# Kernel tuning notes

Measured on AMD Instinct MI355X. Metric: run time of the kernel, lower is better.

Reference implementation:

```python
import jax, jax.numpy as jnp
import numpy as np

N_NODES = 100000
N_EDGES = 1600000
DIM = 128


def setup_inputs() -> dict:
    key = jax.random.key(0)
    k1, k2, k3, k4 = jax.random.split(key, 4)
    x = jax.random.normal(k1, (N_NODES, DIM), dtype=jnp.float32)
    edge_index = jax.random.randint(k2, (2, N_EDGES), 0, N_NODES, dtype=jnp.int64)
    # PyG GCNConv params: Linear weight [out, in] (glorot) and bias [out] (zeros -> use small randn for a non-trivial grad path)
    W = jax.random.normal(k3, (DIM, DIM), dtype=jnp.float32) * (1.0 / np.sqrt(DIM))
    b = jax.random.normal(k4, (DIM,), dtype=jnp.float32) * 0.01
    return {"x": x, "edge_index": edge_index, "W": W, "b": b}


def reference(x, edge_index, W, b):
    # Faithful GCNConv: add self-loops, symmetric deg^-1/2 normalization,
    # linear transform, scatter-add aggregation, bias.
    N = x.shape[0]
    loop = jnp.arange(N, dtype=edge_index.dtype)
    src = jnp.concatenate([edge_index[0], loop])  # [E+N]
    dst = jnp.concatenate([edge_index[1], loop])  # [E+N]

    # degree (with self-loops) on destination nodes
    deg = jax.ops.segment_sum(jnp.ones_like(dst, dtype=x.dtype), dst, num_segments=N)
    dinv = jnp.where(deg > 0, jax.lax.rsqrt(deg), 0.0)
    norm = dinv[src] * dinv[dst]  # [E+N]

    x_lin = x @ W.T  # [N, dim] — PyG applies linear before propagate
    msg = x_lin[src] * norm[:, None]  # [E+N, dim] gather + scale
    out = jax.ops.segment_sum(msg, dst, num_segments=N)  # scatter-add aggregate
    return out + b
```

## Files before the change

### kernel.cpp

```cpp
#include <hip/hip_runtime.h>
#include <hip/hip_bf16.h>


#define DIM 128
#define BINSHIFT 8
#define BINSZ 256
#define NB 391
#define CAPB 8192
#define BUFCAP 40
#define SBLK 128
#define ROUND 2048
#define WSTRIDE 136

typedef __attribute__((ext_vector_type(8))) short short8;
typedef __attribute__((ext_vector_type(4))) float f32x4;
typedef __attribute__((ext_vector_type(4))) unsigned short ushort4v;

__device__ inline unsigned short f2bf(float f) {
    unsigned u = __builtin_bit_cast(unsigned, f);
    return (unsigned short)((u + 0x7FFFu + ((u >> 16) & 1u)) >> 16);
}

__device__ inline void bf8_axpy(uint4 v, float s, float* acc) {
    acc[0] = fmaf(s, __builtin_bit_cast(float, v.x << 16), acc[0]);
    acc[1] = fmaf(s, __builtin_bit_cast(float, v.x & 0xFFFF0000u), acc[1]);
    acc[2] = fmaf(s, __builtin_bit_cast(float, v.y << 16), acc[2]);
    acc[3] = fmaf(s, __builtin_bit_cast(float, v.y & 0xFFFF0000u), acc[3]);
    acc[4] = fmaf(s, __builtin_bit_cast(float, v.z << 16), acc[4]);
    acc[5] = fmaf(s, __builtin_bit_cast(float, v.z & 0xFFFF0000u), acc[5]);
    acc[6] = fmaf(s, __builtin_bit_cast(float, v.w << 16), acc[6]);
    acc[7] = fmaf(s, __builtin_bit_cast(float, v.w & 0xFFFF0000u), acc[7]);
}

__global__ __launch_bounds__(512) void scatter_ms(const int* __restrict__ ei, int E,
                                                  int* __restrict__ binCursor,
                                                  unsigned* __restrict__ binned,
                                                  const float* __restrict__ W,
                                                  unsigned short* __restrict__ wbf) {
    int t = threadIdx.x;
    if ((int)blockIdx.x >= SBLK) {
        int base = ((int)blockIdx.x - SBLK) * 2048 + t * 4;
#pragma unroll
        for (int i = 0; i < 4; ++i) {
            float4 w4 = ((const float4*)W)[base + i];
            ushort4v o; o.x = f2bf(w4.x); o.y = f2bf(w4.y); o.z = f2bf(w4.z); o.w = f2bf(w4.w);
            ((ushort4v*)wbf)[base + i] = o;
        }
        return;
    }

    __shared__ int cnt[NB];
    __shared__ unsigned buf[NB * BUFCAP];
    for (int i = t; i < NB; i += 512) cnt[i] = 0;
    __syncthreads();

    int chunk = (E + SBLK - 1) / SBLK;
    int base = blockIdx.x * chunk;
    int end = min(E, base + chunk);

    for (int rb = base; rb < end; rb += ROUND) {
        int re = min(end, rb + ROUND);
        for (int i = rb + t; i < re; i += 512) {
            int s = ei[i];
            int d = ei[E + i];
            int b = d >> BINSHIFT;
            unsigned p = ((unsigned)(d & (BINSZ - 1)) << 17) | (unsigned)s;
            int pos = atomicAdd(&cnt[b], 1);
            if (pos < BUFCAP) buf[b * BUFCAP + pos] = p;
            else binned[(size_t)b * CAPB + atomicAdd(&binCursor[b], 1)] = p;
        }
        __syncthreads();
        for (int b = t; b < NB; b += 512) {
            int c = min(cnt[b], BUFCAP);
            int full = c & ~15;
            if (full > 0) {
                int gbase = atomicAdd(&binCursor[b], full);
                unsigned* gp = binned + (size_t)b * CAPB + gbase;
                const unsigned* lp = &buf[b * BUFCAP];
                if ((gbase & 3) == 0) {
                    for (int g = 0; g < full; g += 4)
                        *(uint4*)(gp + g) = *(const uint4*)(lp + g);
                } else {
                    for (int g = 0; g < full; ++g) gp[g] = lp[g];
                }
                int rem = c - full;
                for (int j = 0; j < rem; ++j)
                    buf[b * BUFCAP + j] = buf[b * BUFCAP + full + j];
                cnt[b] = rem;
            } else {
                cnt[b] = c;
            }
        }
        __syncthreads();
    }
    for (int b = t; b < NB; b += 512) {
        int c = min(cnt[b], BUFCAP);
        if (c > 0) {
            int gbase = atomicAdd(&binCursor[b], c);
            unsigned* gp = binned + (size_t)b * CAPB + gbase;
            for (int j = 0; j < c; ++j) gp[j] = buf[b * BUFCAP + j];
        }
    }
}

__global__ __launch_bounds__(512) void csr_gemm(const unsigned* __restrict__ binned,
                                                const int* __restrict__ binCursor,
                                                int* __restrict__ col,
                                                int2* __restrict__ rowinfo,
                                                float* __restrict__ dinv,
                                                const float* __restrict__ x,
                                                const unsigned short* __restrict__ wbf,
                                                unsigned short* __restrict__ xlin, int N) {
    __shared__ __align__(16) char smem[8 * 16 * WSTRIDE * 2];
    int t = threadIdx.x;

    if ((int)blockIdx.x < NB) {
        int* ldeg = (int*)smem;
        int* sa   = ldeg + BINSZ;
        int* sb2  = sa + BINSZ;
        int* lcur = sb2 + BINSZ;
        int b = blockIdx.x;
        int s0 = b * CAPB;
        int s1 = s0 + binCursor[b];

        if (t < BINSZ) { ldeg[t] = 0; lcur[t] = 0; }
        __syncthreads();
        for (int i = s0 + t; i < s1; i += 512)
            atomicAdd(&ldeg[binned[i] >> 17], 1);
        __syncthreads();
        if (t < BINSZ) sa[t] = ldeg[t];
        __syncthreads();
        int* src = sa; int* dstp = sb2;
        for (int step = 1; step < BINSZ; step <<= 1) {
            if (t < BINSZ) {
                int v = src[t];
                if (t >= step) v += src[t - step];
                dstp[t] = v;
            }
            __syncthreads();
            int* tmp = src; src = dstp; dstp = tmp;
        }
        if (t < BINSZ) {
            int d = ldeg[t];
            int startoff = src[t] - d;
            int n = (b << BINSHIFT) + t;
            if (n < N) {
                rowinfo[n] = make_int2(s0 + startoff, d);
                dinv[n] = rsqrtf((float)(d + 1));
            }
            dstp[t] = startoff;
        }
        __syncthreads();
        for (int i = s0 + t; i < s1; i += 512) {
            unsigned p = binned[i];
            int li = p >> 17;
            col[s0 + dstp[li] + atomicAdd(&lcur[li], 1)] = (int)(p & 0x1FFFFu);
        }
        return;
    }

    unsigned short* obuf = (unsigned short*)smem;
    int wid = t >> 6, lane = t & 63;
    int m = lane & 15, quad = lane >> 4;
    int row_base = ((int)blockIdx.x - NB) * 128 + wid * 16;

    f32x4 acc[8];
#pragma unroll
    for (int j = 0; j < 8; ++j) acc[j] = (f32x4){0.f, 0.f, 0.f, 0.f};

    int arow = row_base + m;
    if (arow >= N) arow = N - 1;
    const float* xr = x + (size_t)arow * DIM + quad * 8;

#pragma unroll
    for (int kc = 0; kc < 4; ++kc) {
        float4 a0 = *(const float4*)(xr + kc * 32);
        float4 a1 = *(const float4*)(xr + kc * 32 + 4);
        short8 af;
        af[0] = (short)f2bf(a0.x); af[1] = (short)f2bf(a0.y);
        af[2] = (short)f2bf(a0.z); af[3] = (short)f2bf(a0.w);
        af[4] = (short)f2bf(a1.x); af[5] = (short)f2bf(a1.y);
        af[6] = (short)f2bf(a1.z); af[7] = (short)f2bf(a1.w);
#pragma unroll
        for (int jt = 0; jt < 8; ++jt) {
            short8 bf = *(const short8*)&wbf[(jt * 16 + m) * DIM + kc * 32 + quad * 8];
            acc[jt] = __builtin_amdgcn_mfma_f32_16x16x32_bf16(af, bf, acc[jt], 0, 0, 0);
        }
    }

    unsigned short* ob = &obuf[wid * 16 * WSTRIDE];
#pragma unroll
    for (int jt = 0; jt < 8; ++jt)
#pragma unroll
        for (int r = 0; r < 4; ++r)
            ob[(quad * 4 + r) * WSTRIDE + jt * 16 + m] = f2bf(acc[jt][r]);
    __syncthreads();
#pragma unroll
    for (int it = 0; it < 4; ++it) {
        int idx = it * 64 + lane;
        int r = idx >> 4;
        int cb = idx & 15;
        int grow = row_base + r;
        if (grow < N) {
            short8 v = *(const short8*)&ob[r * WSTRIDE + cb * 8];
            *(short8*)(xlin + (size_t)grow * DIM + cb * 8) = v;
        }
    }
}


__global__ __launch_bounds__(256) void aggregate(const unsigned short* __restrict__ xlin,
                                                 const int* __restrict__ col,
                                                 const int2* __restrict__ rowinfo,
                                                 const float* __restrict__ dinv,
                                                 const float* __restrict__ bias,
                                                 float* __restrict__ out, int N) {
    int node = blockIdx.x * 16 + (threadIdx.x >> 4);
    int lane = threadIdx.x & 15;
    if (node >= N) return;

    float di = dinv[node];
    int2 ri = rowinfo[node];
    int r0 = ri.x, r1 = ri.x + ri.y;

    const uint4* xl = (const uint4*)xlin;
    float acc[8] = {};
    bf8_axpy(xl[(size_t)node * 16 + lane], di, acc);

    for (int i = r0; i < r1; i += 4) {
        int rem = r1 - i;
        int s0 = col[i];
        int s1 = col[rem > 1 ? i + 1 : i];
        int s2 = col[rem > 2 ? i + 2 : i];
        int s3 = col[rem > 3 ? i + 3 : i];
        float d0 = dinv[s0];
        float d1 = rem > 1 ? dinv[s1] : 0.f;
        float d2 = rem > 2 ? dinv[s2] : 0.f;
        float d3 = rem > 3 ? dinv[s3] : 0.f;
        uint4 v0 = xl[(size_t)s0 * 16 + lane];
        uint4 v1 = xl[(size_t)s1 * 16 + lane];
        uint4 v2 = xl[(size_t)s2 * 16 + lane];
        uint4 v3 = xl[(size_t)s3 * 16 + lane];
        bf8_axpy(v0, d0, acc);
        bf8_axpy(v1, d1, acc);
        bf8_axpy(v2, d2, acc);
        bf8_axpy(v3, d3, acc);
    }

    const float4* b4 = (const float4*)(bias + lane * 8);
    float4 bl = b4[0], bh = b4[1];
    float4 olo = make_float4(di * acc[0] + bl.x, di * acc[1] + bl.y,
                             di * acc[2] + bl.z, di * acc[3] + bl.w);
    float4 ohi = make_float4(di * acc[4] + bh.x, di * acc[5] + bh.y,
                             di * acc[6] + bh.z, di * acc[7] + bh.w);
    float4* op = (float4*)(out + (size_t)node * DIM + lane * 8);
    op[0] = olo;
    op[1] = ohi;
}


extern "C" void kernel_launch(void* const* d_in, const int* in_sizes, int n_in,
                              void* d_out, int out_size, void* d_ws, size_t ws_size,
                              hipStream_t stream) {
    const float* x    = (const float*)d_in[0];
    const int*   ei   = (const int*)d_in[1];
    const float* W    = (const float*)d_in[2];
    const float* bias = (const float*)d_in[3];
    float* out = (float*)d_out;

    const int N = in_sizes[0] / DIM;
    const int E = in_sizes[1] / 2;

    char* ws = (char*)d_ws;
    size_t off = 0;
    auto alloc = [&](size_t bytes) { size_t o = off; off = (off + bytes + 255) & ~(size_t)255; return o; };
    unsigned short* xlin = (unsigned short*)(ws + alloc((size_t)N * DIM * 2));
    unsigned* binned = (unsigned*)(ws + alloc((size_t)NB * CAPB * 4));
    int*  col      = (int*)  (ws + alloc((size_t)NB * CAPB * 4));
    int2* rowinfo  = (int2*) (ws + alloc((size_t)N * 8));
    float* dinv    = (float*)(ws + alloc((size_t)N * 4));
    int*  binCursor= (int*)  (ws + alloc((size_t)NB * 4 + 256));
    unsigned short* wbf = (unsigned short*)(ws + alloc((size_t)DIM * DIM * 2));

    int GB = (N + 127) / 128;

    hipMemsetAsync(binCursor, 0, (size_t)NB * 4, stream);
    scatter_ms<<<SBLK + 2, 512, 0, stream>>>(ei, E, binCursor, binned, W, wbf);
    csr_gemm<<<NB + GB, 512, 0, stream>>>(binned, binCursor, col, rowinfo, dinv, x, wbf, xlin, N);
    aggregate<<<(N + 15) / 16, 256, 0, stream>>>(xlin, col, rowinfo, dinv, bias, out, N);
}
```

Before: 232.3 us.

## Fuse binning, GEMM, CSR build and aggregation into one cooperative persistent kernel

Replaces the three-kernel pipeline with a single cooperative persistent kernel. Half the blocks bin edges while the other half run the MFMA linear transform. Two grid-wide syncs separate that phase from CSR construction and then from aggregation. The W-to-bf16 conversion moves into a small separate kernel, and the edge binning drops its round-based flushing for a single pass with a smaller shared buffer. This removes launch gaps and overlaps binning with the GEMM, at the cost of grid.sync overhead, a fixed grid size that limits parallelism in aggregation and CSR build, and more edges spilling to global atomics.

```diff
diff --git a/kernel.cpp b/kernel.cpp
--- a/kernel.cpp
+++ b/kernel.cpp
@@ -1,16 +1,17 @@
 #include <hip/hip_runtime.h>
-#include <hip/hip_bf16.h>
-
+#include <hip/hip_cooperative_groups.h>
+
+
+namespace cg = cooperative_groups;
 
 #define DIM 128
 #define BINSHIFT 8
 #define BINSZ 256
 #define NB 391
 #define CAPB 8192
-#define BUFCAP 40
-#define SBLK 128
-#define ROUND 2048
+#define BUFCAP 32
 #define WSTRIDE 136
+#define SMEMSZ 51616
 
 typedef __attribute__((ext_vector_type(8))) short short8;
 typedef __attribute__((ext_vector_type(4))) float f32x4;
@@ -20,242 +21,213 @@
     unsigned u = __builtin_bit_cast(unsigned, f);
     return (unsigned short)((u + 0x7FFFu + ((u >> 16) & 1u)) >> 16);
 }
+__device__ inline float bflo(unsigned u) { return __builtin_bit_cast(float, u << 16); }
+__device__ inline float bfhi(unsigned u) { return __builtin_bit_cast(float, u & 0xFFFF0000u); }
 
 __device__ inline void bf8_axpy(uint4 v, float s, float* acc) {
-    acc[0] = fmaf(s, __builtin_bit_cast(float, v.x << 16), acc[0]);
-    acc[1] = fmaf(s, __builtin_bit_cast(float, v.x & 0xFFFF0000u), acc[1]);
-    acc[2] = fmaf(s, __builtin_bit_cast(float, v.y << 16), acc[2]);
-    acc[3] = fmaf(s, __builtin_bit_cast(float, v.y & 0xFFFF0000u), acc[3]);
-    acc[4] = fmaf(s, __builtin_bit_cast(float, v.z << 16), acc[4]);
-    acc[5] = fmaf(s, __builtin_bit_cast(float, v.z & 0xFFFF0000u), acc[5]);
-    acc[6] = fmaf(s, __builtin_bit_cast(float, v.w << 16), acc[6]);
-    acc[7] = fmaf(s, __builtin_bit_cast(float, v.w & 0xFFFF0000u), acc[7]);
-}
-
-__global__ __launch_bounds__(512) void scatter_ms(const int* __restrict__ ei, int E,
-                                                  int* __restrict__ binCursor,
-                                                  unsigned* __restrict__ binned,
-                                                  const float* __restrict__ W,
-                                                  unsigned short* __restrict__ wbf) {
+    acc[0] = fmaf(s, bflo(v.x), acc[0]);
+    acc[1] = fmaf(s, bfhi(v.x), acc[1]);
+    acc[2] = fmaf(s, bflo(v.y), acc[2]);
+    acc[3] = fmaf(s, bfhi(v.y), acc[3]);
+    acc[4] = fmaf(s, bflo(v.z), acc[4]);
+    acc[5] = fmaf(s, bfhi(v.z), acc[5]);
+    acc[6] = fmaf(s, bflo(v.w), acc[6]);
+    acc[7] = fmaf(s, bfhi(v.w), acc[7]);
+}
+
+__global__ __launch_bounds__(256) void wconv(const float* __restrict__ W,
+                                             unsigned short* __restrict__ wbf) {
+    int base = blockIdx.x * 1024 + threadIdx.x * 4;
+#pragma unroll
+    for (int i = 0; i < 4; ++i) {
+        float4 w4 = ((const float4*)W)[base + i];
+        ushort4v o; o.x = f2bf(w4.x); o.y = f2bf(w4.y); o.z = f2bf(w4.z); o.w = f2bf(w4.w);
+        ((ushort4v*)wbf)[base + i] = o;
+    }
+}
+
+__global__ __launch_bounds__(512, 6) void gcn_mega(
+        const int* __restrict__ ei, int E,
+        int* __restrict__ binCursor, unsigned* __restrict__ binned,
+        int* __restrict__ col, int2* __restrict__ rowinfo, float* __restrict__ dinv,
+        const float* __restrict__ x, const unsigned short* __restrict__ wbf,
+        unsigned short* __restrict__ xlin,
+        const float* __restrict__ bias, float* __restrict__ out,
+        int N, int SB) {
+    __shared__ __align__(16) char smem[SMEMSZ];
+    cg::grid_group grid = cg::this_grid();
     int t = threadIdx.x;
-    if ((int)blockIdx.x >= SBLK) {
-        int base = ((int)blockIdx.x - SBLK) * 2048 + t * 4;
-#pragma unroll
-        for (int i = 0; i < 4; ++i) {
-            float4 w4 = ((const float4*)W)[base + i];
-            ushort4v o; o.x = f2bf(w4.x); o.y = f2bf(w4.y); o.z = f2bf(w4.z); o.w = f2bf(w4.w);
-            ((ushort4v*)wbf)[base + i] = o;
-        }
-        return;
-    }
-
-    __shared__ int cnt[NB];
-    __shared__ unsigned buf[NB * BUFCAP];
-    for (int i = t; i < NB; i += 512) cnt[i] = 0;
-    __syncthreads();
-
-    int chunk = (E + SBLK - 1) / SBLK;
-    int base = blockIdx.x * chunk;
-    int end = min(E, base + chunk);
-
-    for (int rb = base; rb < end; rb += ROUND) {
-        int re = min(end, rb + ROUND);
-        for (int i = rb + t; i < re; i += 512) {
+    int bid = blockIdx.x;
+    int G = gridDim.x;
+
+    if (bid < SB) {
+        int* cnt = (int*)smem;
+        unsigned* sbuf = (unsigned*)(smem + 1568);
+        for (int i = t; i < NB; i += 512) cnt[i] = 0;
+        __syncthreads();
+        int chunk = (E + SB - 1) / SB;
+        int base = bid * chunk, end = min(E, base + chunk);
+        for (int i = base + t; i < end; i += 512) {
             int s = ei[i];
             int d = ei[E + i];
             int b = d >> BINSHIFT;
             unsigned p = ((unsigned)(d & (BINSZ - 1)) << 17) | (unsigned)s;
             int pos = atomicAdd(&cnt[b], 1);
-            if (pos < BUFCAP) buf[b * BUFCAP + pos] = p;
+            if (pos < BUFCAP) sbuf[b * BUFCAP + pos] = p;
             else binned[(size_t)b * CAPB + atomicAdd(&binCursor[b], 1)] = p;
         }
         __syncthreads();
         for (int b = t; b < NB; b += 512) {
             int c = min(cnt[b], BUFCAP);
-            int full = c & ~15;
-            if (full > 0) {
-                int gbase = atomicAdd(&binCursor[b], full);
-                unsigned* gp = binned + (size_t)b * CAPB + gbase;
-                const unsigned* lp = &buf[b * BUFCAP];
-                if ((gbase & 3) == 0) {
-                    for (int g = 0; g < full; g += 4)
-                        *(uint4*)(gp + g) = *(const uint4*)(lp + g);
-                } else {
-                    for (int g = 0; g < full; ++g) gp[g] = lp[g];
-                }
-                int rem = c - full;
-                for (int j = 0; j < rem; ++j)
-                    buf[b * BUFCAP + j] = buf[b * BUFCAP + full + j];
-                cnt[b] = rem;
-            } else {
-                cnt[b] = c;
-            }
-        }
-        __syncthreads();
-    }
-    for (int b = t; b < NB; b += 512) {
-        int c = min(cnt[b], BUFCAP);
-        if (c > 0) {
-            int gbase = atomicAdd(&binCursor[b], c);
-            unsigned* gp = binned + (size_t)b * CAPB + gbase;
-            for (int j = 0; j < c; ++j) gp[j] = buf[b * BUFCAP + j];
-        }
-    }
-}
-
-__global__ __launch_bounds__(512) void csr_gemm(const unsigned* __restrict__ binned,
-                                                const int* __restrict__ binCursor,
-                                                int* __restrict__ col,
-                                                int2* __restrict__ rowinfo,
-                                                float* __restrict__ dinv,
-                                                const float* __restrict__ x,
-                                                const unsigned short* __restrict__ wbf,
-                                                unsigned short* __restrict__ xlin, int N) {
-    __shared__ __align__(16) char smem[8 * 16 * WSTRIDE * 2];
-    int t = threadIdx.x;
-
-    if ((int)blockIdx.x < NB) {
+            if (c > 0) {
+                int gb = atomicAdd(&binCursor[b], c);
+                unsigned* gp = binned + (size_t)b * CAPB + gb;
+                const unsigned* lp = &sbuf[b * BUFCAP];
+                for (int j = 0; j < c; ++j) gp[j] = lp[j];
+            }
+        }
+    } else {
+        unsigned short* obuf = (unsigned short*)smem;
+        int wid = t >> 6, lane = t & 63;
+        int m = lane & 15, quad = lane >> 4;
+        int GBn = (N + 127) >> 7;
+        for (int grp = bid - SB; grp < GBn; grp += (G - SB)) {
+            int row_base = grp * 128 + wid * 16;
+            f32x4 acc[8];
+#pragma unroll
+            for (int j = 0; j < 8; ++j) acc[j] = (f32x4){0.f, 0.f, 0.f, 0.f};
+            int arow = row_base + m;
+            if (arow >= N) arow = N - 1;
+            const float* xr = x + (size_t)arow * DIM + quad * 8;
+#pragma unroll
+            for (int kc = 0; kc < 4; ++kc) {
+                float4 a0 = *(const float4*)(xr + kc * 32);
+                float4 a1 = *(const float4*)(xr + kc * 32 + 4);
+                short8 af;
+                af[0] = (short)f2bf(a0.x); af[1] = (short)f2bf(a0.y);
+                af[2] = (short)f2bf(a0.z); af[3] = (short)f2bf(a0.w);
+                af[4] = (short)f2bf(a1.x); af[5] = (short)f2bf(a1.y);
+                af[6] = (short)f2bf(a1.z); af[7] = (short)f2bf(a1.w);
+#pragma unroll
+                for (int jt = 0; jt < 8; ++jt) {
+                    short8 bf = *(const short8*)&wbf[(jt * 16 + m) * DIM + kc * 32 + quad * 8];
+                    acc[jt] = __builtin_amdgcn_mfma_f32_16x16x32_bf16(af, bf, acc[jt], 0, 0, 0);
+                }
+            }
+            unsigned short* ob = &obuf[wid * 16 * WSTRIDE];
+#pragma unroll
+            for (int jt = 0; jt < 8; ++jt)
+#pragma unroll
+                for (int r = 0; r < 4; ++r)
+                    ob[(quad * 4 + r) * WSTRIDE + jt * 16 + m] = f2bf(acc[jt][r]);
+#pragma unroll
+            for (int it = 0; it < 4; ++it) {
+                int idx = it * 64 + lane;
+                int r = idx >> 4;
+                int cb = idx & 15;
+                int grow = row_base - wid * 16 + (wid * 16 + r);
+                if (grow < N) {
+                    short8 v = *(const short8*)&ob[r * WSTRIDE + cb * 8];
+                    *(short8*)(xlin + (size_t)grow * DIM + cb * 8) = v;
+                }
+            }
+        }
+    }
+    __threadfence();
+    grid.sync();
+
+    {
         int* ldeg = (int*)smem;
-        int* sa   = ldeg + BINSZ;
-        int* sb2  = sa + BINSZ;
+        int* sa = ldeg + BINSZ;
+        int* sb2 = sa + BINSZ;
         int* lcur = sb2 + BINSZ;
-        int b = blockIdx.x;
-        int s0 = b * CAPB;
-        int s1 = s0 + binCursor[b];
-
-        if (t < BINSZ) { ldeg[t] = 0; lcur[t] = 0; }
-        __syncthreads();
-        for (int i = s0 + t; i < s1; i += 512)
-            atomicAdd(&ldeg[binned[i] >> 17], 1);
-        __syncthreads();
-        if (t < BINSZ) sa[t] = ldeg[t];
-        __syncthreads();
-        int* src = sa; int* dstp = sb2;
-        for (int step = 1; step < BINSZ; step <<= 1) {
+        for (int b = bid; b < NB; b += G) {
+            int s0 = b * CAPB;
+            int s1 = s0 + binCursor[b];
+            if (t < BINSZ) { ldeg[t] = 0; lcur[t] = 0; }
+            __syncthreads();
+            for (int i = s0 + t; i < s1; i += 512)
+                atomicAdd(&ldeg[binned[i] >> 17], 1);
+            __syncthreads();
+            if (t < BINSZ) sa[t] = ldeg[t];
+            __syncthreads();
+            int* src = sa; int* dstp = sb2;
+            for (int step = 1; step < BINSZ; step <<= 1) {
+                if (t < BINSZ) {
+                    int v = src[t];
+                    if (t >= step) v += src[t - step];
+                    dstp[t] = v;
+                }
+                __syncthreads();
+                int* tmp = src; src = dstp; dstp = tmp;
+            }
             if (t < BINSZ) {
-                int v = src[t];
-                if (t >= step) v += src[t - step];
-                dstp[t] = v;
-            }
-            __syncthreads();
-            int* tmp = src; src = dstp; dstp = tmp;
-        }
-        if (t < BINSZ) {
-            int d = ldeg[t];
-            int startoff = src[t] - d;
-            int n = (b << BINSHIFT) + t;
-            if (n < N) {
-                rowinfo[n] = make_int2(s0 + startoff, d);
-                dinv[n] = rsqrtf((float)(d + 1));
-            }
-            dstp[t] = startoff;
-        }
-        __syncthreads();
-        for (int i = s0 + t; i < s1; i += 512) {
-            unsigned p = binned[i];
-            int li = p >> 17;
-            col[s0 + dstp[li] + atomicAdd(&lcur[li], 1)] = (int)(p & 0x1FFFFu);
-        }
-        return;
-    }
-
-    unsigned short* obuf = (unsigned short*)smem;
-    int wid = t >> 6, lane = t & 63;
-    int m = lane & 15, quad = lane >> 4;
-    int row_base = ((int)blockIdx.x - NB) * 128 + wid * 16;
-
-    f32x4 acc[8];
-#pragma unroll
-    for (int j = 0; j < 8; ++j) acc[j] = (f32x4){0.f, 0.f, 0.f, 0.f};
-
-    int arow = row_base + m;
-    if (arow >= N) arow = N - 1;
-    const float* xr = x + (size_t)arow * DIM + quad * 8;
-
-#pragma unroll
-    for (int kc = 0; kc < 4; ++kc) {
-        float4 a0 = *(const float4*)(xr + kc * 32);
-        float4 a1 = *(const float4*)(xr + kc * 32 + 4);
-        short8 af;
-        af[0] = (short)f2bf(a0.x); af[1] = (short)f2bf(a0.y);
-        af[2] = (short)f2bf(a0.z); af[3] = (short)f2bf(a0.w);
-        af[4] = (short)f2bf(a1.x); af[5] = (short)f2bf(a1.y);
-        af[6] = (short)f2bf(a1.z); af[7] = (short)f2bf(a1.w);
-#pragma unroll
-        for (int jt = 0; jt < 8; ++jt) {
-            short8 bf = *(const short8*)&wbf[(jt * 16 + m) * DIM + kc * 32 + quad * 8];
-            acc[jt] = __builtin_amdgcn_mfma_f32_16x16x32_bf16(af, bf, acc[jt], 0, 0, 0);
-        }
-    }
-
-    unsigned short* ob = &obuf[wid * 16 * WSTRIDE];
-#pragma unroll
-    for (int jt = 0; jt < 8; ++jt)
-#pragma unroll
-        for (int r = 0; r < 4; ++r)
-            ob[(quad * 4 + r) * WSTRIDE + jt * 16 + m] = f2bf(acc[jt][r]);
-    __syncthreads();
-#pragma unroll
-    for (int it = 0; it < 4; ++it) {
-        int idx = it * 64 + lane;
-        int r = idx >> 4;
-        int cb = idx & 15;
-        int grow = row_base + r;
-        if (grow < N) {
-            short8 v = *(const short8*)&ob[r * WSTRIDE + cb * 8];
-            *(short8*)(xlin + (size_t)grow * DIM + cb * 8) = v;
-        }
-    }
-}
-
-
-__global__ __launch_bounds__(256) void aggregate(const unsigned short* __restrict__ xlin,
-                                                 const int* __restrict__ col,
-                                                 const int2* __restrict__ rowinfo,
-                                                 const float* __restrict__ dinv,
-                                                 const float* __restrict__ bias,
-                                                 float* __restrict__ out, int N) {
-    int node = blockIdx.x * 16 + (threadIdx.x >> 4);
-    int lane = threadIdx.x & 15;
-    if (node >= N) return;
-
-    float di = dinv[node];
-    int2 ri = rowinfo[node];
-    int r0 = ri.x, r1 = ri.x + ri.y;
-
-    const uint4* xl = (const uint4*)xlin;
-    float acc[8] = {};
-    bf8_axpy(xl[(size_t)node * 16 + lane], di, acc);
-
-    for (int i = r0; i < r1; i += 4) {
-        int rem = r1 - i;
-        int s0 = col[i];
-        int s1 = col[rem > 1 ? i + 1 : i];
-        int s2 = col[rem > 2 ? i + 2 : i];
-        int s3 = col[rem > 3 ? i + 3 : i];
-        float d0 = dinv[s0];
-        float d1 = rem > 1 ? dinv[s1] : 0.f;
-        float d2 = rem > 2 ? dinv[s2] : 0.f;
-        float d3 = rem > 3 ? dinv[s3] : 0.f;
-        uint4 v0 = xl[(size_t)s0 * 16 + lane];
-        uint4 v1 = xl[(size_t)s1 * 16 + lane];
-        uint4 v2 = xl[(size_t)s2 * 16 + lane];
-        uint4 v3 = xl[(size_t)s3 * 16 + lane];
-        bf8_axpy(v0, d0, acc);
-        bf8_axpy(v1, d1, acc);
-        bf8_axpy(v2, d2, acc);
-        bf8_axpy(v3, d3, acc);
-    }
-
-    const float4* b4 = (const float4*)(bias + lane * 8);
-    float4 bl = b4[0], bh = b4[1];
-    float4 olo = make_float4(di * acc[0] + bl.x, di * acc[1] + bl.y,
-                             di * acc[2] + bl.z, di * acc[3] + bl.w);
-    float4 ohi = make_float4(di * acc[4] + bh.x, di * acc[5] + bh.y,
-                             di * acc[6] + bh.z, di * acc[7] + bh.w);
-    float4* op = (float4*)(out + (size_t)node * DIM + lane * 8);
-    op[0] = olo;
-    op[1] = ohi;
+                int d = ldeg[t];
+                int startoff = src[t] - d;
+                int n = (b << BINSHIFT) + t;
+                if (n < N) {
+                    rowinfo[n] = make_int2(s0 + startoff, d);
+                    dinv[n] = rsqrtf((float)(d + 1));
+                }
+                dstp[t] = startoff;
+            }
+            __syncthreads();
+            for (int i = s0 + t; i < s1; i += 512) {
+                unsigned p = binned[i];
+                int li = p >> 17;
+                col[s0 + dstp[li] + atomicAdd(&lcur[li], 1)] = (int)(p & 0x1FFFFu);
+            }
+            __syncthreads();
+        }
+    }
+    __threadfence();
+    grid.sync();
+
+    {
+        int lane = t & 15;
+        const uint4* xl = (const uint4*)xlin;
+        int NGRP = (N + 31) >> 5;
+        for (int grp = bid; grp < NGRP; grp += G) {
+            int node = grp * 32 + (t >> 4);
+            if (node >= N) continue;
+            float di = dinv[node];
+            int2 ri = rowinfo[node];
+            int r0 = ri.x, r1 = ri.x + ri.y;
+
+            float acc[8] = {};
+            bf8_axpy(xl[(size_t)node * 16 + lane], di, acc);
+
+            for (int i = r0; i < r1; i += 4) {
+                int rem = r1 - i;
+                int s0 = col[i];
+                int s1 = col[rem > 1 ? i + 1 : i];
+                int s2 = col[rem > 2 ? i + 2 : i];
+                int s3 = col[rem > 3 ? i + 3 : i];
+                float d0 = dinv[s0];
+                float d1 = rem > 1 ? dinv[s1] : 0.f;
+                float d2 = rem > 2 ? dinv[s2] : 0.f;
+                float d3 = rem > 3 ? dinv[s3] : 0.f;
+                uint4 v0 = xl[(size_t)s0 * 16 + lane];
+                uint4 v1 = xl[(size_t)s1 * 16 + lane];
+                uint4 v2 = xl[(size_t)s2 * 16 + lane];
+                uint4 v3 = xl[(size_t)s3 * 16 + lane];
+                bf8_axpy(v0, d0, acc);
+                bf8_axpy(v1, d1, acc);
+                bf8_axpy(v2, d2, acc);
+                bf8_axpy(v3, d3, acc);
+            }
+
+            const float4* b4 = (const float4*)(bias + lane * 8);
+            float4 bl = b4[0], bh = b4[1];
+            float4 olo = make_float4(di * acc[0] + bl.x, di * acc[1] + bl.y,
+                                     di * acc[2] + bl.z, di * acc[3] + bl.w);
+            float4 ohi = make_float4(di * acc[4] + bh.x, di * acc[5] + bh.y,
+                                     di * acc[6] + bh.z, di * acc[7] + bh.w);
+            float4* op = (float4*)(out + (size_t)node * DIM + lane * 8);
+            op[0] = olo;
+            op[1] = ohi;
+        }
+    }
 }
 
 
@@ -268,8 +240,8 @@
     const float* bias = (const float*)d_in[3];
     float* out = (float*)d_out;
 
-    const int N = in_sizes[0] / DIM;
-    const int E = in_sizes[1] / 2;
+    int N = in_sizes[0] / DIM;
+    int E = in_sizes[1] / 2;
 
     char* ws = (char*)d_ws;
     size_t off = 0;
@@ -282,10 +254,21 @@
     int*  binCursor= (int*)  (ws + alloc((size_t)NB * 4 + 256));
     unsigned short* wbf = (unsigned short*)(ws + alloc((size_t)DIM * DIM * 2));
 
-    int GB = (N + 127) / 128;
+    int maxb = 0;
+    hipOccupancyMaxActiveBlocksPerMultiprocessor(&maxb, gcn_mega, 512, 0);
+    if (maxb < 1) maxb = 1;
+    int G = maxb * 256;
+    if (G > 768) G = 768;
+    if (G & 1) --G;
+    if (G < 2) G = 2;
+    int SB = G / 2;
 
     hipMemsetAsync(binCursor, 0, (size_t)NB * 4, stream);
-    scatter_ms<<<SBLK + 2, 512, 0, stream>>>(ei, E, binCursor, binned, W, wbf);
-    csr_gemm<<<NB + GB, 512, 0, stream>>>(binned, binCursor, col, rowinfo, dinv, x, wbf, xlin, N);
-    aggregate<<<(N + 15) / 16, 256, 0, stream>>>(xlin, col, rowinfo, dinv, bias, out, N);
-}
+    wconv<<<4, 256, 0, stream>>>(W, wbf);
+
+    void* args[] = { (void*)&ei, (void*)&E, (void*)&binCursor, (void*)&binned,
+                     (void*)&col, (void*)&rowinfo, (void*)&dinv, (void*)&x,
+                     (void*)&wbf, (void*)&xlin, (void*)&bias, (void*)&out,
+                     (void*)&N, (void*)&SB };
+    hipLaunchCooperativeKernel(gcn_mega, dim3(G), dim3(512), args, 0, stream);
+}
```

Result: slower. 557.7 us (+140.1%).
